# Kernel tuning notes

Measured on AMD Instinct MI355X. Metric: run time of the kernel, lower is better.

Reference implementation:

```python
import jax, jax.numpy as jnp
import numpy as np
from jax.scipy.special import logsumexp


def setup_inputs() -> dict:
    key = jax.random.key(0)
    k1, k2 = jax.random.split(key)
    B, T, V = 128, 128, 32000
    inputs = jax.random.normal(k1, (B, T), dtype=jnp.float32)
    # LDA init stddev = sqrt((1/beta)*(1 - 1/V)) with beta = 1/V
    stddev = ((1.0 / (1.0 / V)) * (1.0 - 1.0 / V)) ** 0.5
    w = jax.random.normal(k2, (T, V), dtype=jnp.float32) * jnp.float32(stddev)
    return {"inputs": inputs, "w": w}


def reference(inputs, w):
    # inputs: (B, T) unnormalized log topic weights; w: (T, V) unnormalized log word dists
    # inference path: no dropout (training=None)
    log_theta = inputs - logsumexp(inputs, axis=1, keepdims=True)   # (B, T)
    log_phi = w - logsumexp(w, axis=1, keepdims=True)               # (T, V)
    # log-domain matmul: z[b, v] = logsumexp_t(log_theta[b, t] + log_phi[t, v])
    z = logsumexp(log_theta[:, :, None] + log_phi[None, :, :], axis=1)  # (B, V)
    return z
```

## Files before the change

kernel.cpp:

```cpp
#include <hip/hip_runtime.h>
#include <math.h>


constexpr int B = 128;
constexpr int T = 128;
constexpr int V = 32000;
constexpr int VC = 64;
constexpr int KPARTS = 4;
constexpr int PART = V / KPARTS;

constexpr int WS_EA = 0;
constexpr int WS_PM = 8192;
constexpr int WS_PS = WS_PM + T * KPARTS;
constexpr int WS_GT = WS_PS + T * KPARTS;

typedef __attribute__((ext_vector_type(8))) short bf16x8;
typedef __attribute__((ext_vector_type(4))) float f32x4;
typedef __attribute__((ext_vector_type(4))) unsigned u32x4;

__device__ inline unsigned short f2bf(float f) {
    union { float f; unsigned u; } x; x.f = f;
    unsigned u = x.u + 0x7fff + ((x.u >> 16) & 1);
    return (unsigned short)(u >> 16);
}

__device__ inline int swz_word(int row, int tp) {
    return (((tp >> 2) ^ (row & 15)) << 2) | (tp & 3);
}

__global__ __launch_bounds__(256) void k_stage1(const float* __restrict__ inp,
                                                const float* __restrict__ w,
                                                float* __restrict__ pm,
                                                float* __restrict__ ps,
                                                float* __restrict__ gt_out,
                                                unsigned* __restrict__ Ea) {
    __shared__ float sh[B * (T + 1)];
    __shared__ float gts[T];
    const int tid = threadIdx.x;

    if (blockIdx.x != 0) {
        const int bid = blockIdx.x - 1;
        const int t = bid >> 2;
        const int part = bid & 3;
        const float4* row = (const float4*)(w + (size_t)t * V + (size_t)part * PART);

        float m = -INFINITY;
        for (int i = tid; i < PART / 4; i += 256) {
            float4 x4 = row[i];
            m = fmaxf(fmaxf(m, fmaxf(x4.x, x4.y)), fmaxf(x4.z, x4.w));
        }
        float* sm = sh;
        sm[tid] = m;
        __syncthreads();
        for (int off = 128; off > 0; off >>= 1) {
            if (tid < off) sm[tid] = fmaxf(sm[tid], sm[tid + off]);
            __syncthreads();
        }
        const float M = sm[0];

        float s = 0.f;
        for (int i = tid; i < PART / 4; i += 256) {
            float4 x4 = row[i];
            s += __expf(x4.x - M) + __expf(x4.y - M) + __expf(x4.z - M) + __expf(x4.w - M);
        }
        float* ss = sh + 256;
        ss[tid] = s;
        __syncthreads();
        for (int off = 128; off > 0; off >>= 1) {
            if (tid < off) ss[tid] += ss[tid + off];
            __syncthreads();
        }
        if (tid == 0) { pm[bid] = M; ps[bid] = ss[0]; }
        return;
    }

    #pragma unroll
    for (int k = 0; k < 16; ++k) {
        int i4 = tid + k * 256;
        float4 x = ((const float4*)inp)[i4];
        int r = i4 >> 5, c = (i4 & 31) * 4;
        float* dst = &sh[r * 129 + c];
        dst[0] = x.x; dst[1] = x.y; dst[2] = x.z; dst[3] = x.w;
    }
    __syncthreads();

    if (tid < B) {
        const int b = tid;
        const float* row = &sh[b * 129];
        float m = -INFINITY;
        for (int t = 0; t < T; ++t) m = fmaxf(m, row[t]);
        float s = 0.f;
        for (int t = 0; t < T; ++t) s += __expf(row[t] - m);
        sh[b * 129 + 128] = m + logf(s);
    }
    __syncthreads();

    if (tid < T) {
        const int t = tid;
        float g = -INFINITY;
        for (int b = 0; b < B; ++b) g = fmaxf(g, sh[b * 129 + t] - sh[b * 129 + 128]);
        gts[t] = g;
        gt_out[t] = g;
    }
    __syncthreads();

    if (tid < B) {
        const int b = tid;
        const float li = sh[b * 129 + 128];
        unsigned pk[64];
        #pragma unroll
        for (int tp = 0; tp < 64; ++tp) {
            float e0 = __expf(sh[b * 129 + 2 * tp]     - li - gts[2 * tp]);
            float e1 = __expf(sh[b * 129 + 2 * tp + 1] - li - gts[2 * tp + 1]);
            pk[tp] = (unsigned)f2bf(e0) | ((unsigned)f2bf(e1) << 16);
        }
        unsigned* row = (unsigned*)&sh[b * 129];
        #pragma unroll
        for (int tp = 0; tp < 64; ++tp) row[swz_word(b, tp)] = pk[tp];
    }
    __syncthreads();

    #pragma unroll
    for (int k = 0; k < 32; ++k) {
        int d = tid + k * 256;
        int b = d >> 6, wsw = d & 63;
        Ea[d] = ((unsigned*)&sh[b * 129])[wsw];
    }
}

__global__ __launch_bounds__(256) void k_main(const float* __restrict__ w,
                                              const float* __restrict__ pm,
                                              const float* __restrict__ ps,
                                              const float* __restrict__ gt,
                                              const unsigned* __restrict__ Ea_g,
                                              float* __restrict__ out) {
    __shared__ unsigned EaL[B * 64];
    __shared__ unsigned EwL[VC * 64];
    __shared__ float cs[T];
    __shared__ float mu[VC];
    __shared__ float pmT[VC][17];

    const int tid = threadIdx.x;
    const int vbase = blockIdx.x * VC;
    const int v4 = tid & 15;
    const int tq = tid >> 4;

    f32x4 wr[8];
    {
        const float* wp = w + (size_t)(tq * 8) * V + vbase + v4 * 4;
        #pragma unroll
        for (int i = 0; i < 8; ++i)
            wr[i] = *(const f32x4*)(wp + (size_t)i * V);
    }

    if (tid < T) {
        const int t = tid;
        float M = pm[t * KPARTS];
        #pragma unroll
        for (int p = 1; p < KPARTS; ++p) M = fmaxf(M, pm[t * KPARTS + p]);
        float S = 0.f;
        #pragma unroll
        for (int p = 0; p < KPARTS; ++p) S += ps[t * KPARTS + p] * __expf(pm[t * KPARTS + p] - M);
        cs[t] = gt[t] - (M + logf(S));
    }

    {
        const float4* src = (const float4*)Ea_g;
        float4* dst = (float4*)EaL;
        #pragma unroll
        for (int k = 0; k < 8; ++k) dst[tid + k * 256] = src[tid + k * 256];
    }
    __syncthreads();

    {
        float p0 = -INFINITY, p1 = -INFINITY, p2 = -INFINITY, p3 = -INFINITY;
        #pragma unroll
        for (int i = 0; i < 8; ++i) {
            const float cc = cs[tq * 8 + i];
            p0 = fmaxf(p0, wr[i][0] + cc);
            p1 = fmaxf(p1, wr[i][1] + cc);
            p2 = fmaxf(p2, wr[i][2] + cc);
            p3 = fmaxf(p3, wr[i][3] + cc);
        }
        pmT[v4 * 4 + 0][tq] = p0;
        pmT[v4 * 4 + 1][tq] = p1;
        pmT[v4 * 4 + 2][tq] = p2;
        pmT[v4 * 4 + 3][tq] = p3;
    }
    __syncthreads();
    if (tid < VC) {
        float m = pmT[tid][0];
        #pragma unroll
        for (int r = 1; r < 16; ++r) m = fmaxf(m, pmT[tid][r]);
        mu[tid] = m;
    }
    __syncthreads();

    {
        #pragma unroll
        for (int c = 0; c < 4; ++c) {
            const int v = v4 * 4 + c;
            const float m_ = mu[v];
            unsigned pk[4];
            #pragma unroll
            for (int p2 = 0; p2 < 4; ++p2) {
                float e0 = __expf(wr[2 * p2][c]     + cs[tq * 8 + 2 * p2]     - m_);
                float e1 = __expf(wr[2 * p2 + 1][c] + cs[tq * 8 + 2 * p2 + 1] - m_);
                pk[p2] = (unsigned)f2bf(e0) | ((unsigned)f2bf(e1) << 16);
            }
            *(u32x4*)&EwL[v * 64 + ((tq ^ (v & 15)) << 2)] = (u32x4){pk[0], pk[1], pk[2], pk[3]};
        }
    }
    __syncthreads();

    const int lane = tid & 63;
    const int wave = tid >> 6;
    const int wb = (wave >> 1) * 64;
    const int wv = (wave & 1) * 32;
    const int r = lane & 15;
    const int g = lane >> 4;

    f32x4 acc[4][2];
    #pragma unroll
    for (int m = 0; m < 4; ++m)
        #pragma unroll
        for (int n = 0; n < 2; ++n) acc[m][n] = (f32x4){0.f, 0.f, 0.f, 0.f};

    #pragma unroll
    for (int kk = 0; kk < 4; ++kk) {
        const int grp = kk * 4 + g;
        bf16x8 af[4], bfr[2];
        #pragma unroll
        for (int m = 0; m < 4; ++m) {
            int bb = wb + m * 16 + r;
            af[m] = *(const bf16x8*)((const char*)EaL + bb * 256 + ((grp ^ (bb & 15)) << 4));
        }
        #pragma unroll
        for (int n = 0; n < 2; ++n) {
            int vv = wv + n * 16 + r;
            bfr[n] = *(const bf16x8*)((const char*)EwL + vv * 256 + ((grp ^ (vv & 15)) << 4));
        }
        #pragma unroll
        for (int m = 0; m < 4; ++m)
            #pragma unroll
            for (int n = 0; n < 2; ++n)
                acc[m][n] = __builtin_amdgcn_mfma_f32_16x16x32_bf16(af[m], bfr[n], acc[m][n], 0, 0, 0);
    }

    #pragma unroll
    for (int m = 0; m < 4; ++m) {
        int bb = wb + m * 16 + g * 4;
        #pragma unroll
        for (int n = 0; n < 2; ++n) {
            float muv = mu[wv + n * 16 + r];
            size_t col = (size_t)(vbase + wv + n * 16 + r);
            #pragma unroll
            for (int j = 0; j < 4; ++j)
                out[(size_t)(bb + j) * V + col] = muv + __logf(acc[m][n][j]);
        }
    }
}

extern "C" void kernel_launch(void* const* d_in, const int* in_sizes, int n_in,
                              void* d_out, int out_size, void* d_ws, size_t ws_size,
                              hipStream_t stream) {
    const float* inp = (const float*)d_in[0];
    const float* w   = (const float*)d_in[1];
    float* out = (float*)d_out;
    unsigned* ws = (unsigned*)d_ws;

    unsigned* Ea = ws + WS_EA;
    float* pm = (float*)(ws + WS_PM);
    float* ps = (float*)(ws + WS_PS);
    float* gt = (float*)(ws + WS_GT);

    k_stage1<<<dim3(T * KPARTS + 1), dim3(256), 0, stream>>>(inp, w, pm, ps, gt, Ea);
    k_main<<<dim3(V / VC), dim3(256), 0, stream>>>(w, pm, ps, gt, Ea, out);
}
```

Measured before the change: 30.08 us.

## Read A fragments directly from global and shrink stage-1 LDS footprint

```diff
diff --git a/kernel.cpp b/kernel.cpp
--- a/kernel.cpp
+++ b/kernel.cpp
@@ -24,17 +24,14 @@
     return (unsigned short)(u >> 16);
 }
 
-__device__ inline int swz_word(int row, int tp) {
-    return (((tp >> 2) ^ (row & 15)) << 2) | (tp & 3);
-}
-
 __global__ __launch_bounds__(256) void k_stage1(const float* __restrict__ inp,
                                                 const float* __restrict__ w,
                                                 float* __restrict__ pm,
                                                 float* __restrict__ ps,
                                                 float* __restrict__ gt_out,
                                                 unsigned* __restrict__ Ea) {
-    __shared__ float sh[B * (T + 1)];
+    __shared__ float si[32][129];
+    __shared__ float lse_b[B];
     __shared__ float gts[T];
     const int tid = threadIdx.x;
 
@@ -44,12 +41,14 @@
         const int part = bid & 3;
         const float4* row = (const float4*)(w + (size_t)t * V + (size_t)part * PART);
 
+        float* sm = &si[0][0];
+        float* ss = &si[4][0];
+
         float m = -INFINITY;
         for (int i = tid; i < PART / 4; i += 256) {
             float4 x4 = row[i];
             m = fmaxf(fmaxf(m, fmaxf(x4.x, x4.y)), fmaxf(x4.z, x4.w));
         }
-        float* sm = sh;
         sm[tid] = m;
         __syncthreads();
         for (int off = 128; off > 0; off >>= 1) {
@@ -63,7 +62,6 @@
             float4 x4 = row[i];
             s += __expf(x4.x - M) + __expf(x4.y - M) + __expf(x4.z - M) + __expf(x4.w - M);
         }
-        float* ss = sh + 256;
         ss[tid] = s;
         __syncthreads();
         for (int off = 128; off > 0; off >>= 1) {
@@ -74,57 +72,68 @@
         return;
     }
 
-    #pragma unroll
-    for (int k = 0; k < 16; ++k) {
-        int i4 = tid + k * 256;
-        float4 x = ((const float4*)inp)[i4];
-        int r = i4 >> 5, c = (i4 & 31) * 4;
-        float* dst = &sh[r * 129 + c];
-        dst[0] = x.x; dst[1] = x.y; dst[2] = x.z; dst[3] = x.w;
-    }
-    __syncthreads();
-
-    if (tid < B) {
-        const int b = tid;
-        const float* row = &sh[b * 129];
-        float m = -INFINITY;
-        for (int t = 0; t < T; ++t) m = fmaxf(m, row[t]);
-        float s = 0.f;
-        for (int t = 0; t < T; ++t) s += __expf(row[t] - m);
-        sh[b * 129 + 128] = m + logf(s);
-    }
-    __syncthreads();
-
-    if (tid < T) {
-        const int t = tid;
-        float g = -INFINITY;
-        for (int b = 0; b < B; ++b) g = fmaxf(g, sh[b * 129 + t] - sh[b * 129 + 128]);
-        gts[t] = g;
-        gt_out[t] = g;
-    }
-    __syncthreads();
-
-    if (tid < B) {
-        const int b = tid;
-        const float li = sh[b * 129 + 128];
-        unsigned pk[64];
-        #pragma unroll
-        for (int tp = 0; tp < 64; ++tp) {
-            float e0 = __expf(sh[b * 129 + 2 * tp]     - li - gts[2 * tp]);
-            float e1 = __expf(sh[b * 129 + 2 * tp + 1] - li - gts[2 * tp + 1]);
-            pk[tp] = (unsigned)f2bf(e0) | ((unsigned)f2bf(e1) << 16);
-        }
-        unsigned* row = (unsigned*)&sh[b * 129];
-        #pragma unroll
-        for (int tp = 0; tp < 64; ++tp) row[swz_word(b, tp)] = pk[tp];
-    }
-    __syncthreads();
-
-    #pragma unroll
-    for (int k = 0; k < 32; ++k) {
-        int d = tid + k * 256;
-        int b = d >> 6, wsw = d & 63;
-        Ea[d] = ((unsigned*)&sh[b * 129])[wsw];
+    const int row8 = tid >> 3;
+    const int sub = tid & 7;
+
+    float greg = -INFINITY;
+    for (int c = 0; c < 4; ++c) {
+        #pragma unroll
+        for (int k = 0; k < 4; ++k) {
+            int i4 = tid + k * 256;
+            float4 x = ((const float4*)inp)[c * 1024 + i4];
+            int r = i4 >> 5, col = (i4 & 31) * 4;
+            float* dst = &si[r][col];
+            dst[0] = x.x; dst[1] = x.y; dst[2] = x.z; dst[3] = x.w;
+        }
+        __syncthreads();
+
+        {
+            const float* row = si[row8];
+            float m = -INFINITY;
+            #pragma unroll
+            for (int j = 0; j < 16; ++j) m = fmaxf(m, row[sub * 16 + j]);
+            #pragma unroll
+            for (int d = 1; d < 8; d <<= 1) m = fmaxf(m, __shfl_xor(m, d, 64));
+            float s = 0.f;
+            #pragma unroll
+            for (int j = 0; j < 16; ++j) s += __expf(row[sub * 16 + j] - m);
+            #pragma unroll
+            for (int d = 1; d < 8; d <<= 1) s += __shfl_xor(s, d, 64);
+            if (sub == 0) lse_b[c * 32 + row8] = m + logf(s);
+        }
+        __syncthreads();
+
+        if (tid < T) {
+            #pragma unroll 8
+            for (int r = 0; r < 32; ++r)
+                greg = fmaxf(greg, si[r][tid] - lse_b[c * 32 + r]);
+        }
+        __syncthreads();
+    }
+    if (tid < T) { gts[tid] = greg; gt_out[tid] = greg; }
+    __syncthreads();
+
+    for (int c = 0; c < 4; ++c) {
+        #pragma unroll
+        for (int k = 0; k < 4; ++k) {
+            int i4 = tid + k * 256;
+            float4 x = ((const float4*)inp)[c * 1024 + i4];
+            int r = i4 >> 5, col = (i4 & 31) * 4;
+            float* dst = &si[r][col];
+            dst[0] = x.x; dst[1] = x.y; dst[2] = x.z; dst[3] = x.w;
+        }
+        __syncthreads();
+
+        const int b = c * 32 + row8;
+        const float li = lse_b[b];
+        #pragma unroll
+        for (int k = 0; k < 8; ++k) {
+            int tp = sub * 8 + k;
+            float e0 = __expf(si[row8][2 * tp]     - li - gts[2 * tp]);
+            float e1 = __expf(si[row8][2 * tp + 1] - li - gts[2 * tp + 1]);
+            Ea[b * 64 + tp] = (unsigned)f2bf(e0) | ((unsigned)f2bf(e1) << 16);
+        }
+        __syncthreads();
     }
 }
 
@@ -134,11 +143,11 @@
                                               const float* __restrict__ gt,
                                               const unsigned* __restrict__ Ea_g,
                                               float* __restrict__ out) {
-    __shared__ unsigned EaL[B * 64];
     __shared__ unsigned EwL[VC * 64];
     __shared__ float cs[T];
     __shared__ float mu[VC];
-    __shared__ float pmT[VC][17];
+
+    float* pmT = (float*)EwL;
 
     const int tid = threadIdx.x;
     const int vbase = blockIdx.x * VC;
@@ -162,13 +171,6 @@
         #pragma unroll
         for (int p = 0; p < KPARTS; ++p) S += ps[t * KPARTS + p] * __expf(pm[t * KPARTS + p] - M);
         cs[t] = gt[t] - (M + logf(S));
-    }
-
-    {
-        const float4* src = (const float4*)Ea_g;
-        float4* dst = (float4*)EaL;
-        #pragma unroll
-        for (int k = 0; k < 8; ++k) dst[tid + k * 256] = src[tid + k * 256];
     }
     __syncthreads();
 
@@ -182,16 +184,16 @@
             p2 = fmaxf(p2, wr[i][2] + cc);
             p3 = fmaxf(p3, wr[i][3] + cc);
         }
-        pmT[v4 * 4 + 0][tq] = p0;
-        pmT[v4 * 4 + 1][tq] = p1;
-        pmT[v4 * 4 + 2][tq] = p2;
-        pmT[v4 * 4 + 3][tq] = p3;
+        pmT[(v4 * 4 + 0) * 17 + tq] = p0;
+        pmT[(v4 * 4 + 1) * 17 + tq] = p1;
+        pmT[(v4 * 4 + 2) * 17 + tq] = p2;
+        pmT[(v4 * 4 + 3) * 17 + tq] = p3;
     }
     __syncthreads();
     if (tid < VC) {
-        float m = pmT[tid][0];
-        #pragma unroll
-        for (int r = 1; r < 16; ++r) m = fmaxf(m, pmT[tid][r]);
+        float m = pmT[tid * 17];
+        #pragma unroll
+        for (int r = 1; r < 16; ++r) m = fmaxf(m, pmT[tid * 17 + r]);
         mu[tid] = m;
     }
     __syncthreads();
@@ -233,7 +235,7 @@
         #pragma unroll
         for (int m = 0; m < 4; ++m) {
             int bb = wb + m * 16 + r;
-            af[m] = *(const bf16x8*)((const char*)EaL + bb * 256 + ((grp ^ (bb & 15)) << 4));
+            af[m] = *(const bf16x8*)((const char*)Ea_g + bb * 256 + grp * 16);
         }
         #pragma unroll
         for (int n = 0; n < 2; ++n) {
```

Measured after the change: 32.44 us. +7.8%, slower.
